# Kernel tuning notes

Hardware: AMD Instinct MI355X
Metric: run time of the kernel (lower is better)

Reference implementation:

```python
import jax, jax.numpy as jnp
import numpy as np
import math

B, T, D, H = 4, 1024, 1024, 16
HD = D // H  # 64
ROPE_BASE = 10000.0


def _apply_rope(q, k):
    # q, k: [B, H, T, HD]; interleaved even/odd rotation as in RotaryEmbedding
    t_len = q.shape[2]
    half = q.shape[-1] // 2
    inv_freq = 1.0 / (ROPE_BASE ** (jnp.arange(half, dtype=jnp.float32) / half))
    freqs = jnp.arange(t_len, dtype=jnp.float32)[:, None] * inv_freq  # [T, half]
    cos = jnp.cos(freqs)
    sin = jnp.sin(freqs)

    def rot(u):
        u1 = u[..., ::2]   # even lanes
        u2 = u[..., 1::2]  # odd lanes
        e = u1 * cos - u2 * sin
        o = u2 * cos + u1 * sin
        return jnp.stack([e, o], axis=-1).reshape(u.shape)

    return rot(q), rot(k)


def _split_heads(x):
    b, t, d = x.shape
    return x.reshape(b, t, H, HD).transpose(0, 2, 1, 3)  # [B,H,T,HD]


def _mha(x, Wq, bq, Wk, bk, Wv, bv, Wo, bo, mask):
    q = _split_heads(jnp.einsum('btd,ed->bte', x, Wq) + bq)
    k = _split_heads(jnp.einsum('btd,ed->bte', x, Wk) + bk)
    v = _split_heads(jnp.einsum('btd,ed->bte', x, Wv) + bv)
    q, k = _apply_rope(q, k)
    scores = jnp.einsum('bhtd,bhsd->bhts', q.astype(jnp.float32),
                        k.astype(jnp.float32)) / math.sqrt(HD)
    scores = jnp.where(mask, scores, -jnp.inf)
    attn = jax.nn.softmax(scores, axis=-1).astype(v.dtype)
    ctx = jnp.einsum('bhts,bhsd->bhtd', attn.astype(jnp.float32),
                     v.astype(jnp.float32)).astype(v.dtype)
    ctx = ctx.transpose(0, 2, 1, 3).reshape(x.shape[0], x.shape[1], D)
    z = jnp.einsum('btd,ed->bte', ctx, Wo) + bo
    return z


def setup_inputs() -> dict:
    key = jax.random.key(0)
    ks = jax.random.split(key, 9)
    s = 0.02
    inp = {
        'x':  jax.random.normal(ks[0], (B, T, D), jnp.float32),
        'Wq': jax.random.normal(ks[1], (D, D), jnp.float32) * s,
        'bq': jax.random.normal(ks[2], (D,), jnp.float32) * s,
        'Wk': jax.random.normal(ks[3], (D, D), jnp.float32) * s,
        'bk': jax.random.normal(ks[4], (D,), jnp.float32) * s,
        'Wv': jax.random.normal(ks[5], (D, D), jnp.float32) * s,
        'bv': jax.random.normal(ks[6], (D,), jnp.float32) * s,
        'Wo': jax.random.normal(ks[7], (D, D), jnp.float32) * s,
        'bo': jax.random.normal(ks[8], (D,), jnp.float32) * s,
        'mask': jnp.tril(jnp.ones((T, T), dtype=bool))[None, None],  # causal
    }
    return inp


def reference(x, Wq, bq, Wk, bk, Wv, bv, Wo, bo, mask):
    return _mha(x, Wq, bq, Wk, bk, Wv, bv, Wo, bo, mask)
```

## Files before the change

### kernel.cpp

```cpp
#include <hip/hip_runtime.h>


#define T_SEQ 1024
#define NH    16
#define HDIM  64
#define DM    1024
#define MTOK  4096

typedef __attribute__((ext_vector_type(8))) short short8;
typedef __attribute__((ext_vector_type(4))) float f32x4;
typedef unsigned short u16;

__device__ __forceinline__ u16 f2bf(float f) {
  unsigned int u = __builtin_bit_cast(unsigned int, f);
  u += 0x7fffu + ((u >> 16) & 1u);
  return (u16)(u >> 16);
}

__device__ __forceinline__ void gll16(const void* g, void* l) {
  __builtin_amdgcn_global_load_lds(
      (const __attribute__((address_space(1))) unsigned int*)(unsigned long long)(g),
      (__attribute__((address_space(3))) unsigned int*)(unsigned int)(unsigned long long)(l),
      16, 0, 0);
}

__global__ void prep_kernel(const float* __restrict__ x,
                            const float* __restrict__ Wq, const float* __restrict__ Wk,
                            const float* __restrict__ Wv, const float* __restrict__ Wo,
                            u16* __restrict__ xb, u16* __restrict__ wall,
                            float* __restrict__ ctab, float* __restrict__ stab) {
  const int bid = blockIdx.x, tid = threadIdx.x;
  if (bid < 8192) {
    const float* src;
    u16* dst;
    int i;
    if (bid < 4096) {
      src = x; dst = xb; i = bid * 256 + tid;
    } else {
      const int w = (bid - 4096) >> 10;
      src = w == 0 ? Wq : w == 1 ? Wk : w == 2 ? Wv : Wo;
      dst = wall + (size_t)w * (DM * DM);
      i = ((bid - 4096) & 1023) * 256 + tid;
    }
    float4 f = ((const float4*)src)[i];
    unsigned long long pk = (unsigned long long)f2bf(f.x)
                          | ((unsigned long long)f2bf(f.y) << 16)
                          | ((unsigned long long)f2bf(f.z) << 32)
                          | ((unsigned long long)f2bf(f.w) << 48);
    ((unsigned long long*)dst)[i] = pk;
  } else {
    const int idx = (bid - 8192) * 256 + tid;
    const int t = idx >> 5, i = idx & 31;
    float inv = powf(10000.f, -(float)i * (1.0f / 32.0f));
    float f = (float)t * inv;
    ctab[idx] = cosf(f);
    stab[idx] = sinf(f);
  }
}

template<int BM, int BN, int AI, int BI, int MI, int NJ>
__device__ __forceinline__ void gemm_pipe2(
    const u16* __restrict__ A, const u16* __restrict__ Bw,
    int m0, int n0, u16* As, u16* Bs, f32x4 acc[MI][NJ]) {
  const int tid = threadIdx.x, lane = tid & 63, wave = tid >> 6;
  const int wr = wave >> 1, wc = wave & 1;
  const int srcswz = ((lane & 7) ^ (lane >> 3)) * 8;
  const int NT = DM / 64;

#define STAGE2(t, b)                                                         \
  do {                                                                       \
    _Pragma("unroll") for (int i = 0; i < AI; ++i) {                         \
      const int q = (wave * AI + i) * 64 + lane;                             \
      gll16(&A[(size_t)(m0 + (q >> 3)) * DM + (t) * 64 + srcswz],            \
            &As[(b) * BM * 64 + q * 8]);                                     \
    }                                                                        \
    _Pragma("unroll") for (int i = 0; i < BI; ++i) {                         \
      const int q = (wave * BI + i) * 64 + lane;                             \
      gll16(&Bw[(size_t)(n0 + (q >> 3)) * DM + (t) * 64 + srcswz],           \
            &Bs[(b) * BN * 64 + q * 8]);                                     \
    }                                                                        \
  } while (0)

  STAGE2(0, 0);
  __syncthreads();
  int buf = 0;
  const int arow0 = wr * (BM / 2) + (lane & 15);
  const int brow0 = wc * (BN / 2) + (lane & 15);
  const int c0 = (((lane >> 4)) ^ (lane & 7)) * 8;
  const int c1 = ((4 + (lane >> 4)) ^ (lane & 7)) * 8;
  for (int t = 0; t < NT; ++t) {
    if (t + 1 < NT) STAGE2(t + 1, buf ^ 1);
    short8 af[MI][2], bf[NJ][2];
#pragma unroll
    for (int i = 0; i < MI; ++i) {
      const int r = buf * BM * 64 + (arow0 + i * 16) * 64;
      af[i][0] = *(const short8*)&As[r + c0];
      af[i][1] = *(const short8*)&As[r + c1];
    }
#pragma unroll
    for (int j = 0; j < NJ; ++j) {
      const int r = buf * BN * 64 + (brow0 + j * 16) * 64;
      bf[j][0] = *(const short8*)&Bs[r + c0];
      bf[j][1] = *(const short8*)&Bs[r + c1];
    }
#pragma unroll
    for (int i = 0; i < MI; ++i)
#pragma unroll
      for (int j = 0; j < NJ; ++j) {
        acc[i][j] = __builtin_amdgcn_mfma_f32_16x16x32_bf16(af[i][0], bf[j][0], acc[i][j], 0, 0, 0);
        acc[i][j] = __builtin_amdgcn_mfma_f32_16x16x32_bf16(af[i][1], bf[j][1], acc[i][j], 0, 0, 0);
      }
    __syncthreads();
    buf ^= 1;
  }
#undef STAGE2
}

__global__ __launch_bounds__(256, 2) void qkv_kernel(
    const u16* __restrict__ xb, const u16* __restrict__ wqkv,
    const float* __restrict__ bq, const float* __restrict__ bk, const float* __restrict__ bv,
    const float* __restrict__ ctab, const float* __restrict__ stab,
    u16* __restrict__ qbuf, u16* __restrict__ kbuf, u16* __restrict__ vt) {
  __shared__ __align__(16) u16 As[2 * 128 * 64];
  __shared__ __align__(16) u16 Bs[2 * 192 * 64];
  const int m0 = blockIdx.y * 128;
  const int n0 = blockIdx.x * 192;
  f32x4 acc[4][6];
#pragma unroll
  for (int i = 0; i < 4; ++i)
#pragma unroll
    for (int j = 0; j < 6; ++j)
#pragma unroll
      for (int r = 0; r < 4; ++r) acc[i][j][r] = 0.f;
  gemm_pipe2<128, 192, 4, 6, 4, 6>(xb, wqkv, m0, n0, As, Bs, acc);

  const int lane = threadIdx.x & 63, wave = threadIdx.x >> 6;
  const int wr = wave >> 1, wc = wave & 1;
#pragma unroll
  for (int i = 0; i < 4; ++i) {
#pragma unroll
    for (int j = 0; j < 6; ++j) {
      const int e = n0 + wc * 96 + j * 16 + (lane & 15);
      const int mode = e >> 10;
      const float* bias = mode == 0 ? bq : (mode == 1 ? bk : bv);
      const float bval = bias[e & 1023];
      const int h = (e >> 6) & 15, hd = e & 63;
#pragma unroll
      for (int r = 0; r < 4; ++r) {
        const int m = m0 + wr * 64 + i * 16 + ((lane >> 4) * 4) + r;
        const int b = m >> 10, t = m & 1023;
        float v = acc[i][j][r] + bval;
        if (mode < 2) {
          float p = __shfl_xor(v, 1);
          const int fi = hd >> 1;
          const float cc = ctab[t * 32 + fi], ss = stab[t * 32 + fi];
          v = (hd & 1) ? (v * cc + p * ss) : (v * cc - p * ss);
          u16* dst = mode == 0 ? qbuf : kbuf;
          dst[(((size_t)(b * NH + h) * T_SEQ + t) << 6) + hd] = f2bf(v);
        } else {
          vt[(((size_t)(b * NH + h) * HDIM + hd) << 10) + t] = f2bf(v);
        }
      }
    }
  }
}

__global__ __launch_bounds__(256) void attn_kernel(
    const u16* __restrict__ qbuf, const u16* __restrict__ kbuf,
    const u16* __restrict__ vtb, u16* __restrict__ ctx) {
  __shared__ __align__(16) u16 Ks[2][64 * 64];
  __shared__ __align__(16) u16 Vs[2][64 * 64];
  __shared__ __align__(16) u16 Psm[4][16 * 64];
  const int bh = blockIdx.x;
  const int b = bh >> 4, h = bh & 15;
  const int tid = threadIdx.x, lane = tid & 63, wave = tid >> 6;
  const u16* Qp = qbuf + (size_t)bh * T_SEQ * HDIM;
  const u16* Kp = kbuf + (size_t)bh * T_SEQ * HDIM;
  const u16* Vp = vtb + (size_t)bh * HDIM * T_SEQ;
  u16* Pw = &Psm[wave][0];

  const int srow = tid >> 3;
  const int schx = ((tid & 7) ^ (srow & 7)) * 8;
  const int lx = lane & 7;

#define STG(kvt, bb)                                                            \
  do {                                                                          \
    _Pragma("unroll") for (int c = 0; c < 2; ++c) {                             \
      const int rr = c * 32 + srow;                                             \
      gll16(&Kp[(kvt) * 4096 + rr * 64 + schx], &Ks[bb][c * 2048 + tid * 8]);   \
      gll16(&Vp[(size_t)rr * T_SEQ + (kvt) * 64 + schx], &Vs[bb][c * 2048 + tid * 8]); \
    }                                                                           \
  } while (0)

  for (int phase = 0; phase < 2; ++phase) {
    const int qt = phase ? (15 - (int)blockIdx.y) : (int)blockIdx.y;
    const int q0 = qt * 64;
    const int nkv = qt + 1;
    const int qrow = q0 + wave * 16 + (lane & 15);
    const short8 qf0 = *(const short8*)&Qp[qrow * 64 + ((lane >> 4) * 8)];
    const short8 qf1 = *(const short8*)&Qp[qrow * 64 + 32 + ((lane >> 4) * 8)];

    f32x4 acc_o[4];
    float m_r[4], l_r[4];
#pragma unroll
    for (int i = 0; i < 4; ++i) {
#pragma unroll
      for (int r = 0; r < 4; ++r) acc_o[i][r] = 0.f;
      m_r[i] = -__builtin_inff();
      l_r[i] = 0.f;
    }

    __syncthreads();
    STG(0, 0);
    int cur = 0;

    for (int kvt = 0; kvt < nkv; ++kvt) {
      __syncthreads();
      if (kvt + 1 < nkv) STG(kvt + 1, cur ^ 1);

      f32x4 sacc[4];
#pragma unroll
      for (int cb = 0; cb < 4; ++cb) {
#pragma unroll
        for (int r = 0; r < 4; ++r) sacc[cb][r] = 0.f;
        const int krow = cb * 16 + (lane & 15);
        const short8 kf0 = *(const short8*)&Ks[cur][krow * 64 + (((lane >> 4) ^ lx) * 8)];
        const short8 kf1 = *(const short8*)&Ks[cur][krow * 64 + (((4 + (lane >> 4)) ^ lx) * 8)];
        sacc[cb] = __builtin_amdgcn_mfma_f32_16x16x32_bf16(qf0, kf0, sacc[cb], 0, 0, 0);
        sacc[cb] = __builtin_amdgcn_mfma_f32_16x16x32_bf16(qf1, kf1, sacc[cb], 0, 0, 0);
      }
      const int trow_base = q0 + wave * 16 + ((lane >> 4) * 4);
#pragma unroll
      for (int cb = 0; cb < 4; ++cb) {
        const int scol = kvt * 64 + cb * 16 + (lane & 15);
#pragma unroll
        for (int r = 0; r < 4; ++r) {
          float sv = sacc[cb][r] * 0.125f;
          sacc[cb][r] = (scol > trow_base + r) ? -__builtin_inff() : sv;
        }
      }
      float mt[4];
#pragma unroll
      for (int r = 0; r < 4; ++r)
        mt[r] = fmaxf(fmaxf(sacc[0][r], sacc[1][r]), fmaxf(sacc[2][r], sacc[3][r]));
#pragma unroll
      for (int off = 1; off < 16; off <<= 1)
#pragma unroll
        for (int r = 0; r < 4; ++r) mt[r] = fmaxf(mt[r], __shfl_xor(mt[r], off));
      float sf[4], lt[4];
#pragma unroll
      for (int r = 0; r < 4; ++r) {
        const float mn = fmaxf(m_r[r], mt[r]);
        sf[r] = __expf(m_r[r] - mn);
        m_r[r] = mn;
        lt[r] = 0.f;
      }
#pragma unroll
      for (int cb = 0; cb < 4; ++cb)
#pragma unroll
        for (int r = 0; r < 4; ++r) {
          const float p = __expf(sacc[cb][r] - m_r[r]);
          sacc[cb][r] = p;
          lt[r] += p;
        }
#pragma unroll
      for (int off = 1; off < 16; off <<= 1)
#pragma unroll
        for (int r = 0; r < 4; ++r) lt[r] += __shfl_xor(lt[r], off);
#pragma unroll
      for (int r = 0; r < 4; ++r) l_r[r] = l_r[r] * sf[r] + lt[r];
#pragma unroll
      for (int hb = 0; hb < 4; ++hb)
#pragma unroll
        for (int r = 0; r < 4; ++r) acc_o[hb][r] *= sf[r];

#pragma unroll
      for (int cb = 0; cb < 4; ++cb)
#pragma unroll
        for (int r = 0; r < 4; ++r) {
          const int prow = (lane >> 4) * 4 + r;
          Pw[prow * 64 + ((cb * 16 + (lane & 15)) ^ ((prow & 7) << 3))] = f2bf(sacc[cb][r]);
        }

      const int prr = lane & 15;
#pragma unroll
      for (int kc = 0; kc < 2; ++kc) {
        const short8 pf = *(const short8*)&Pw[prr * 64 + (((kc * 4 + (lane >> 4)) ^ lx) * 8)];
#pragma unroll
        for (int hb = 0; hb < 4; ++hb) {
          const int vrow = hb * 16 + (lane & 15);
          const short8 vf = *(const short8*)&Vs[cur][vrow * 64 + (((kc * 4 + (lane >> 4)) ^ lx) * 8)];
          acc_o[hb] = __builtin_amdgcn_mfma_f32_16x16x32_bf16(pf, vf, acc_o[hb], 0, 0, 0);
        }
      }
      cur ^= 1;
    }

#pragma unroll
    for (int hb = 0; hb < 4; ++hb) {
      const int hd = hb * 16 + (lane & 15);
#pragma unroll
      for (int r = 0; r < 4; ++r) {
        const int t = q0 + wave * 16 + ((lane >> 4) * 4) + r;
        const float v = acc_o[hb][r] / l_r[r];
        ctx[((size_t)(b * T_SEQ + t) * NH + h) * HDIM + hd] = f2bf(v);
      }
    }
  }
#undef STG
}

__global__ __launch_bounds__(256, 2) void oproj_kernel(
    const u16* __restrict__ ctx, const u16* __restrict__ Wob,
    const float* __restrict__ bo, float* __restrict__ out) {
  __shared__ __align__(16) u16 As[2 * 64 * 64];
  __shared__ __align__(16) u16 Bs[2 * 128 * 64];
  const int m0 = blockIdx.y * 64, n0 = blockIdx.x * 128;
  f32x4 acc[2][4];
#pragma unroll
  for (int i = 0; i < 2; ++i)
#pragma unroll
    for (int j = 0; j < 4; ++j)
#pragma unroll
      for (int r = 0; r < 4; ++r) acc[i][j][r] = 0.f;
  gemm_pipe2<64, 128, 2, 4, 2, 4>(ctx, Wob, m0, n0, As, Bs, acc);
  const int lane = threadIdx.x & 63, wave = threadIdx.x >> 6;
  const int wr = wave >> 1, wc = wave & 1;
#pragma unroll
  for (int i = 0; i < 2; ++i)
#pragma unroll
    for (int j = 0; j < 4; ++j) {
      const int e = n0 + wc * 64 + j * 16 + (lane & 15);
      const float bval = bo[e];
#pragma unroll
      for (int r = 0; r < 4; ++r) {
        const int m = m0 + wr * 32 + i * 16 + ((lane >> 4) * 4) + r;
        out[(size_t)m * DM + e] = acc[i][j][r] + bval;
      }
    }
}

extern "C" void kernel_launch(void* const* d_in, const int* in_sizes, int n_in,
                              void* d_out, int out_size, void* d_ws, size_t ws_size,
                              hipStream_t stream) {
  const float* x  = (const float*)d_in[0];
  const float* Wq = (const float*)d_in[1];
  const float* bq = (const float*)d_in[2];
  const float* Wk = (const float*)d_in[3];
  const float* bk = (const float*)d_in[4];
  const float* Wv = (const float*)d_in[5];
  const float* bv = (const float*)d_in[6];
  const float* Wo = (const float*)d_in[7];
  const float* bo = (const float*)d_in[8];

  char* w = (char*)d_ws;
  u16* xb   = (u16*)(w);
  u16* wall = (u16*)(w + (8ull << 20));
  u16* wob  = (u16*)(w + (14ull << 20));
  u16* qb   = (u16*)(w + (16ull << 20));
  u16* kb   = (u16*)(w + (24ull << 20));
  u16* vtb  = (u16*)(w + (32ull << 20));
  u16* ctxb = (u16*)(w + (40ull << 20));
  float* ctab = (float*)(w + (48ull << 20));
  float* stab = ctab + T_SEQ * 32;

  prep_kernel<<<dim3(8192 + 128), 256, 0, stream>>>(x, Wq, Wk, Wv, Wo, xb, wall, ctab, stab);
  qkv_kernel<<<dim3(3 * DM / 192, MTOK / 128), 256, 0, stream>>>(
      xb, wall, bq, bk, bv, ctab, stab, qb, kb, vtb);
  attn_kernel<<<dim3(64, 8), 256, 0, stream>>>(qb, kb, vtb, ctxb);
  oproj_kernel<<<dim3(DM / 128, MTOK / 64), 256, 0, stream>>>(ctxb, wob, bo, (float*)d_out);
}
```

Measured before the change: 109.9 us.

## Replace double-buffered GEMM mainloop with 4-stage vmcnt pipeline and 512-thread tiles

Rewrites the shared GEMM mainloop to use K=32 slices with a four-buffer ring, three loads in flight, and explicit vmcnt waits plus a single barrier per iteration instead of two-stage double buffering with full syncthreads. Both projection kernels move to 512 threads (8 waves in a 2x4 grid). QKV tiles grow to 128x384 and o-proj tiles to 128x128, with a new swizzled LDS layout that packs two rows per 64-element line. The aim is to hide global-load latency and raise data reuse per block, at the cost of fewer blocks (more wave-quantization risk) and heavier reliance on hand-coded waitcnt correctness.

```diff
diff --git a/kernel.cpp b/kernel.cpp
--- a/kernel.cpp
+++ b/kernel.cpp
@@ -22,6 +22,13 @@
       (const __attribute__((address_space(1))) unsigned int*)(unsigned long long)(g),
       (__attribute__((address_space(3))) unsigned int*)(unsigned int)(unsigned long long)(l),
       16, 0, 0);
+}
+
+template<int N> __device__ __forceinline__ void waitvm() {
+  if constexpr (N == 8)      asm volatile("s_waitcnt vmcnt(8)" ::: "memory");
+  else if constexpr (N == 4) asm volatile("s_waitcnt vmcnt(4)" ::: "memory");
+  else if constexpr (N == 2) asm volatile("s_waitcnt vmcnt(2)" ::: "memory");
+  else                       asm volatile("s_waitcnt vmcnt(0)" ::: "memory");
 }
 
 __global__ void prep_kernel(const float* __restrict__ x,
@@ -58,73 +65,76 @@
   }
 }
 
-template<int BM, int BN, int AI, int BI, int MI, int NJ>
-__device__ __forceinline__ void gemm_pipe2(
+template<int BM, int BN, int AL, int BL, int MI, int NJ>
+__device__ __forceinline__ void gemm_pipe4(
     const u16* __restrict__ A, const u16* __restrict__ Bw,
     int m0, int n0, u16* As, u16* Bs, f32x4 acc[MI][NJ]) {
   const int tid = threadIdx.x, lane = tid & 63, wave = tid >> 6;
-  const int wr = wave >> 1, wc = wave & 1;
-  const int srcswz = ((lane & 7) ^ (lane >> 3)) * 8;
-  const int NT = DM / 64;
-
-#define STAGE2(t, b)                                                         \
-  do {                                                                       \
-    _Pragma("unroll") for (int i = 0; i < AI; ++i) {                         \
-      const int q = (wave * AI + i) * 64 + lane;                             \
-      gll16(&A[(size_t)(m0 + (q >> 3)) * DM + (t) * 64 + srcswz],            \
-            &As[(b) * BM * 64 + q * 8]);                                     \
-    }                                                                        \
-    _Pragma("unroll") for (int i = 0; i < BI; ++i) {                         \
-      const int q = (wave * BI + i) * 64 + lane;                             \
-      gll16(&Bw[(size_t)(n0 + (q >> 3)) * DM + (t) * 64 + srcswz],           \
-            &Bs[(b) * BN * 64 + q * 8]);                                     \
-    }                                                                        \
-  } while (0)
-
-  STAGE2(0, 0);
-  __syncthreads();
-  int buf = 0;
-  const int arow0 = wr * (BM / 2) + (lane & 15);
-  const int brow0 = wc * (BN / 2) + (lane & 15);
-  const int c0 = (((lane >> 4)) ^ (lane & 7)) * 8;
-  const int c1 = ((4 + (lane >> 4)) ^ (lane & 7)) * 8;
+  const int wr = wave >> 2, wc = wave & 3;
+  const int NT = DM / 32;
+
+  auto STG = [&](int t, int b) {
+#pragma unroll
+    for (int l = 0; l < AL; ++l) {
+      const int idx = l * 512 + tid, r = idx >> 3, c = (idx & 7) ^ (r & 7);
+      gll16(&A[(size_t)(m0 + 2 * r + (c >> 2)) * DM + t * 32 + (c & 3) * 8],
+            &As[b * (BM * 32) + idx * 8]);
+    }
+#pragma unroll
+    for (int l = 0; l < BL; ++l) {
+      const int idx = l * 512 + tid, r = idx >> 3, c = (idx & 7) ^ (r & 7);
+      gll16(&Bw[(size_t)(n0 + 2 * r + (c >> 2)) * DM + t * 32 + (c & 3) * 8],
+            &Bs[b * (BN * 32) + idx * 8]);
+    }
+  };
+
+  STG(0, 0); STG(1, 1); STG(2, 2);
+
+  const int mrow = lane & 15, q = lane >> 4;
+  int aoff[MI], boff[NJ];
+#pragma unroll
+  for (int i = 0; i < MI; ++i) {
+    const int m = wr * (MI * 16) + i * 16 + mrow, r = m >> 1;
+    const int p = (((m & 1) << 2) + q) ^ (r & 7);
+    aoff[i] = r * 64 + p * 8;
+  }
+#pragma unroll
+  for (int j = 0; j < NJ; ++j) {
+    const int n = wc * (NJ * 16) + j * 16 + mrow, r = n >> 1;
+    const int p = (((n & 1) << 2) + q) ^ (r & 7);
+    boff[j] = r * 64 + p * 8;
+  }
+
   for (int t = 0; t < NT; ++t) {
-    if (t + 1 < NT) STAGE2(t + 1, buf ^ 1);
-    short8 af[MI][2], bf[NJ][2];
-#pragma unroll
-    for (int i = 0; i < MI; ++i) {
-      const int r = buf * BM * 64 + (arow0 + i * 16) * 64;
-      af[i][0] = *(const short8*)&As[r + c0];
-      af[i][1] = *(const short8*)&As[r + c1];
-    }
-#pragma unroll
-    for (int j = 0; j < NJ; ++j) {
-      const int r = buf * BN * 64 + (brow0 + j * 16) * 64;
-      bf[j][0] = *(const short8*)&Bs[r + c0];
-      bf[j][1] = *(const short8*)&Bs[r + c1];
-    }
+    if (t < NT - 2)       waitvm<2 * (AL + BL)>();
+    else if (t == NT - 2) waitvm<AL + BL>();
+    else                  waitvm<0>();
+    asm volatile("s_waitcnt lgkmcnt(0)" ::: "memory");
+    __builtin_amdgcn_s_barrier();
+    if (t + 3 < NT) STG(t + 3, (t + 3) & 3);
+    const int boa = (t & 3) * (BM * 32), bob = (t & 3) * (BN * 32);
+    short8 af[MI], bf[NJ];
+#pragma unroll
+    for (int i = 0; i < MI; ++i) af[i] = *(const short8*)&As[boa + aoff[i]];
+#pragma unroll
+    for (int j = 0; j < NJ; ++j) bf[j] = *(const short8*)&Bs[bob + boff[j]];
 #pragma unroll
     for (int i = 0; i < MI; ++i)
 #pragma unroll
-      for (int j = 0; j < NJ; ++j) {
-        acc[i][j] = __builtin_amdgcn_mfma_f32_16x16x32_bf16(af[i][0], bf[j][0], acc[i][j], 0, 0, 0);
-        acc[i][j] = __builtin_amdgcn_mfma_f32_16x16x32_bf16(af[i][1], bf[j][1], acc[i][j], 0, 0, 0);
-      }
-    __syncthreads();
-    buf ^= 1;
-  }
-#undef STAGE2
-}
-
-__global__ __launch_bounds__(256, 2) void qkv_kernel(
+      for (int j = 0; j < NJ; ++j)
+        acc[i][j] = __builtin_amdgcn_mfma_f32_16x16x32_bf16(af[i], bf[j], acc[i][j], 0, 0, 0);
+  }
+}
+
+__global__ __launch_bounds__(512, 2) void qkv_kernel(
     const u16* __restrict__ xb, const u16* __restrict__ wqkv,
     const float* __restrict__ bq, const float* __restrict__ bk, const float* __restrict__ bv,
     const float* __restrict__ ctab, const float* __restrict__ stab,
     u16* __restrict__ qbuf, u16* __restrict__ kbuf, u16* __restrict__ vt) {
-  __shared__ __align__(16) u16 As[2 * 128 * 64];
-  __shared__ __align__(16) u16 Bs[2 * 192 * 64];
+  __shared__ __align__(16) u16 As[4 * 128 * 32];
+  __shared__ __align__(16) u16 Bs[4 * 384 * 32];
   const int m0 = blockIdx.y * 128;
-  const int n0 = blockIdx.x * 192;
+  const int n0 = blockIdx.x * 384;
   f32x4 acc[4][6];
 #pragma unroll
   for (int i = 0; i < 4; ++i)
@@ -132,10 +142,10 @@
     for (int j = 0; j < 6; ++j)
 #pragma unroll
       for (int r = 0; r < 4; ++r) acc[i][j][r] = 0.f;
-  gemm_pipe2<128, 192, 4, 6, 4, 6>(xb, wqkv, m0, n0, As, Bs, acc);
+  gemm_pipe4<128, 384, 1, 3, 4, 6>(xb, wqkv, m0, n0, As, Bs, acc);
 
   const int lane = threadIdx.x & 63, wave = threadIdx.x >> 6;
-  const int wr = wave >> 1, wc = wave & 1;
+  const int wr = wave >> 2, wc = wave & 3;
 #pragma unroll
   for (int i = 0; i < 4; ++i) {
 #pragma unroll
@@ -310,31 +320,31 @@
 #undef STG
 }
 
-__global__ __launch_bounds__(256, 2) void oproj_kernel(
+__global__ __launch_bounds__(512, 2) void oproj_kernel(
     const u16* __restrict__ ctx, const u16* __restrict__ Wob,
     const float* __restrict__ bo, float* __restrict__ out) {
-  __shared__ __align__(16) u16 As[2 * 64 * 64];
-  __shared__ __align__(16) u16 Bs[2 * 128 * 64];
-  const int m0 = blockIdx.y * 64, n0 = blockIdx.x * 128;
-  f32x4 acc[2][4];
-#pragma unroll
-  for (int i = 0; i < 2; ++i)
-#pragma unroll
-    for (int j = 0; j < 4; ++j)
+  __shared__ __align__(16) u16 As[4 * 128 * 32];
+  __shared__ __align__(16) u16 Bs[4 * 128 * 32];
+  const int m0 = blockIdx.y * 128, n0 = blockIdx.x * 128;
+  f32x4 acc[4][2];
+#pragma unroll
+  for (int i = 0; i < 4; ++i)
+#pragma unroll
+    for (int j = 0; j < 2; ++j)
 #pragma unroll
       for (int r = 0; r < 4; ++r) acc[i][j][r] = 0.f;
-  gemm_pipe2<64, 128, 2, 4, 2, 4>(ctx, Wob, m0, n0, As, Bs, acc);
+  gemm_pipe4<128, 128, 1, 1, 4, 2>(ctx, Wob, m0, n0, As, Bs, acc);
   const int lane = threadIdx.x & 63, wave = threadIdx.x >> 6;
-  const int wr = wave >> 1, wc = wave & 1;
-#pragma unroll
-  for (int i = 0; i < 2; ++i)
-#pragma unroll
-    for (int j = 0; j < 4; ++j) {
-      const int e = n0 + wc * 64 + j * 16 + (lane & 15);
+  const int wr = wave >> 2, wc = wave & 3;
+#pragma unroll
+  for (int i = 0; i < 4; ++i)
+#pragma unroll
+    for (int j = 0; j < 2; ++j) {
+      const int e = n0 + wc * 32 + j * 16 + (lane & 15);
       const float bval = bo[e];
 #pragma unroll
       for (int r = 0; r < 4; ++r) {
-        const int m = m0 + wr * 32 + i * 16 + ((lane >> 4) * 4) + r;
+        const int m = m0 + wr * 64 + i * 16 + ((lane >> 4) * 4) + r;
         out[(size_t)m * DM + e] = acc[i][j][r] + bval;
       }
     }
@@ -365,8 +375,8 @@
   float* stab = ctab + T_SEQ * 32;
 
   prep_kernel<<<dim3(8192 + 128), 256, 0, stream>>>(x, Wq, Wk, Wv, Wo, xb, wall, ctab, stab);
-  qkv_kernel<<<dim3(3 * DM / 192, MTOK / 128), 256, 0, stream>>>(
+  qkv_kernel<<<dim3(3 * DM / 384, MTOK / 128), 512, 0, stream>>>(
       xb, wall, bq, bk, bv, ctab, stab, qb, kb, vtb);
   attn_kernel<<<dim3(64, 8), 256, 0, stream>>>(qb, kb, vtb, ctxb);
-  oproj_kernel<<<dim3(DM / 128, MTOK / 64), 256, 0, stream>>>(ctxb, wob, bo, (float*)d_out);
-}
+  oproj_kernel<<<dim3(DM / 128, MTOK / 128), 512, 0, stream>>>(ctxb, wob, bo, (float*)d_out);
+}
```

Measured after the change: 118.6 us. +7.8%, slower.

## Use exp2 softmax, MFMA row sums, diagonal-only masking, and M-fastest GEMM grid order

Applied to the files above, without the earlier changes.

Attention now folds the 1/sqrt(d)·log2(e) scale into the scores and uses exp2f. The causal mask is applied only on the diagonal KV tile. The running row sum is accumulated by an extra MFMA of P against a ones vector instead of cross-lane shuffle reductions. The QKV and output-projection GEMMs use a 1D grid ordered M-fastest so that neighbouring blocks share weight tiles in cache. The row sum is now taken from bf16-rounded probabilities, which slightly changes numerics.

```diff
diff --git a/kernel.cpp b/kernel.cpp
--- a/kernel.cpp
+++ b/kernel.cpp
@@ -123,8 +123,9 @@
     u16* __restrict__ qbuf, u16* __restrict__ kbuf, u16* __restrict__ vt) {
   __shared__ __align__(16) u16 As[2 * 128 * 64];
   __shared__ __align__(16) u16 Bs[2 * 192 * 64];
-  const int m0 = blockIdx.y * 128;
-  const int n0 = blockIdx.x * 192;
+  const int lin = blockIdx.x;
+  const int m0 = (lin & 31) * 128;
+  const int n0 = (lin >> 5) * 192;
   f32x4 acc[4][6];
 #pragma unroll
   for (int i = 0; i < 4; ++i)
@@ -178,10 +179,15 @@
   const u16* Kp = kbuf + (size_t)bh * T_SEQ * HDIM;
   const u16* Vp = vtb + (size_t)bh * HDIM * T_SEQ;
   u16* Pw = &Psm[wave][0];
+  const float SC = 0.18033688f;
 
   const int srow = tid >> 3;
   const int schx = ((tid & 7) ^ (srow & 7)) * 8;
   const int lx = lane & 7;
+
+  short8 onesf;
+#pragma unroll
+  for (int i = 0; i < 8; ++i) onesf[i] = (short)0x3F80;
 
 #define STG(kvt, bb)                                                            \
   do {                                                                          \
@@ -200,14 +206,14 @@
     const short8 qf0 = *(const short8*)&Qp[qrow * 64 + ((lane >> 4) * 8)];
     const short8 qf1 = *(const short8*)&Qp[qrow * 64 + 32 + ((lane >> 4) * 8)];
 
-    f32x4 acc_o[4];
-    float m_r[4], l_r[4];
+    f32x4 acc_o[4], accl;
+    float m_r[4];
 #pragma unroll
     for (int i = 0; i < 4; ++i) {
 #pragma unroll
       for (int r = 0; r < 4; ++r) acc_o[i][r] = 0.f;
+      accl[i] = 0.f;
       m_r[i] = -__builtin_inff();
-      l_r[i] = 0.f;
     }
 
     __syncthreads();
@@ -229,15 +235,20 @@
         sacc[cb] = __builtin_amdgcn_mfma_f32_16x16x32_bf16(qf0, kf0, sacc[cb], 0, 0, 0);
         sacc[cb] = __builtin_amdgcn_mfma_f32_16x16x32_bf16(qf1, kf1, sacc[cb], 0, 0, 0);
       }
-      const int trow_base = q0 + wave * 16 + ((lane >> 4) * 4);
-#pragma unroll
-      for (int cb = 0; cb < 4; ++cb) {
-        const int scol = kvt * 64 + cb * 16 + (lane & 15);
-#pragma unroll
-        for (int r = 0; r < 4; ++r) {
-          float sv = sacc[cb][r] * 0.125f;
-          sacc[cb][r] = (scol > trow_base + r) ? -__builtin_inff() : sv;
+      if (kvt == qt) {
+        const int trow_base = q0 + wave * 16 + ((lane >> 4) * 4);
+#pragma unroll
+        for (int cb = 0; cb < 4; ++cb) {
+          const int scol = kvt * 64 + cb * 16 + (lane & 15);
+#pragma unroll
+          for (int r = 0; r < 4; ++r)
+            sacc[cb][r] = (scol > trow_base + r) ? -__builtin_inff() : sacc[cb][r] * SC;
         }
+      } else {
+#pragma unroll
+        for (int cb = 0; cb < 4; ++cb)
+#pragma unroll
+          for (int r = 0; r < 4; ++r) sacc[cb][r] *= SC;
       }
       float mt[4];
 #pragma unroll
@@ -247,28 +258,19 @@
       for (int off = 1; off < 16; off <<= 1)
 #pragma unroll
         for (int r = 0; r < 4; ++r) mt[r] = fmaxf(mt[r], __shfl_xor(mt[r], off));
-      float sf[4], lt[4];
+      float sf[4];
 #pragma unroll
       for (int r = 0; r < 4; ++r) {
         const float mn = fmaxf(m_r[r], mt[r]);
-        sf[r] = __expf(m_r[r] - mn);
+        sf[r] = exp2f(m_r[r] - mn);
         m_r[r] = mn;
-        lt[r] = 0.f;
       }
 #pragma unroll
       for (int cb = 0; cb < 4; ++cb)
 #pragma unroll
-        for (int r = 0; r < 4; ++r) {
-          const float p = __expf(sacc[cb][r] - m_r[r]);
-          sacc[cb][r] = p;
-          lt[r] += p;
-        }
-#pragma unroll
-      for (int off = 1; off < 16; off <<= 1)
-#pragma unroll
-        for (int r = 0; r < 4; ++r) lt[r] += __shfl_xor(lt[r], off);
-#pragma unroll
-      for (int r = 0; r < 4; ++r) l_r[r] = l_r[r] * sf[r] + lt[r];
+        for (int r = 0; r < 4; ++r) sacc[cb][r] = exp2f(sacc[cb][r] - m_r[r]);
+#pragma unroll
+      for (int r = 0; r < 4; ++r) accl[r] *= sf[r];
 #pragma unroll
       for (int hb = 0; hb < 4; ++hb)
 #pragma unroll
@@ -286,6 +288,7 @@
 #pragma unroll
       for (int kc = 0; kc < 2; ++kc) {
         const short8 pf = *(const short8*)&Pw[prr * 64 + (((kc * 4 + (lane >> 4)) ^ lx) * 8)];
+        accl = __builtin_amdgcn_mfma_f32_16x16x32_bf16(pf, onesf, accl, 0, 0, 0);
 #pragma unroll
         for (int hb = 0; hb < 4; ++hb) {
           const int vrow = hb * 16 + (lane & 15);
@@ -302,7 +305,7 @@
 #pragma unroll
       for (int r = 0; r < 4; ++r) {
         const int t = q0 + wave * 16 + ((lane >> 4) * 4) + r;
-        const float v = acc_o[hb][r] / l_r[r];
+        const float v = acc_o[hb][r] / accl[r];
         ctx[((size_t)(b * T_SEQ + t) * NH + h) * HDIM + hd] = f2bf(v);
       }
     }
@@ -315,7 +318,9 @@
     const float* __restrict__ bo, float* __restrict__ out) {
   __shared__ __align__(16) u16 As[2 * 64 * 64];
   __shared__ __align__(16) u16 Bs[2 * 128 * 64];
-  const int m0 = blockIdx.y * 64, n0 = blockIdx.x * 128;
+  const int lin = blockIdx.x;
+  const int m0 = (lin & 63) * 64;
+  const int n0 = (lin >> 6) * 128;
   f32x4 acc[2][4];
 #pragma unroll
   for (int i = 0; i < 2; ++i)
@@ -365,8 +370,8 @@
   float* stab = ctab + T_SEQ * 32;
 
   prep_kernel<<<dim3(8192 + 128), 256, 0, stream>>>(x, Wq, Wk, Wv, Wo, xb, wall, ctab, stab);
-  qkv_kernel<<<dim3(3 * DM / 192, MTOK / 128), 256, 0, stream>>>(
+  qkv_kernel<<<dim3(512), 256, 0, stream>>>(
       xb, wall, bq, bk, bv, ctab, stab, qb, kb, vtb);
   attn_kernel<<<dim3(64, 8), 256, 0, stream>>>(qb, kb, vtb, ctxb);
-  oproj_kernel<<<dim3(DM / 128, MTOK / 64), 256, 0, stream>>>(ctxb, wob, bo, (float*)d_out);
-}
+  oproj_kernel<<<dim3(512), 256, 0, stream>>>(ctxb, wob, bo, (float*)d_out);
+}
```

After: 110.6 us. Within noise of the previous version (+0.6%).
